# Optimization experiments

Hardware: AMD Instinct MI355X
Metric: run time of the kernel (lower is better)

The kernel has to match this reference:

```python
import jax, jax.numpy as jnp
import numpy as np

# NF4 16-level codebook (bitsandbytes values)
NF4_CODEBOOK = jnp.array([
    -1.0, -0.6961928009986877, -0.5250730514526367, -0.39491748809814453,
    -0.28444138169288635, -0.18477343022823334, -0.09105003625154495, 0.0,
    0.07958029955625534, 0.16093020141124725, 0.24611230194568634,
    0.33791524171829224, 0.44070982933044434, 0.5626170039176941,
    0.7229568362236328, 1.0], dtype=jnp.float32)

GROUP = 64      # quant_group_size for NF4
R = 16          # LoRA rank
ALPHA = 16      # lora_alpha -> scaling = ALPHA / R = 1.0
E, H, I, T, TOPK = 8, 2048, 1024, 512, 2


def nf4_dequant_gkn(packed, scales, K, N):
    """packed: [E, K//2, N] uint8-valued ints (two 4-bit codes per byte along K).
    scales: [E, K//GROUP, N] float32 per-group absmax. Returns [E, K, N] fp32."""
    e = packed.shape[0]
    lo = packed & 15
    hi = (packed >> 4) & 15
    codes = jnp.stack([lo, hi], axis=2).reshape(e, K, N)      # interleave along K
    w = NF4_CODEBOOK[codes]                                    # [E, K, N]
    w = w.reshape(e, K // GROUP, GROUP, N) * scales[:, :, None, :]
    return w.reshape(e, K, N)


def setup_inputs() -> dict:
    key = jax.random.key(0)
    ks = jax.random.split(key, 16)
    lora_std = 1.0 / np.sqrt(H)
    return {
        "x": jax.random.normal(ks[0], (T, H), jnp.float32),
        "topk_idx": jax.random.randint(ks[1], (T, TOPK), 0, E, jnp.int32),
        "topk_w": jax.random.uniform(ks[2], (T, TOPK), jnp.float32),
        "gate_packed": jax.random.randint(ks[3], (E, H // 2, I), 0, 256, jnp.int32),
        "gate_scales": jax.random.uniform(ks[4], (E, H // GROUP, I), jnp.float32) * 0.02,
        "up_packed": jax.random.randint(ks[5], (E, H // 2, I), 0, 256, jnp.int32),
        "up_scales": jax.random.uniform(ks[6], (E, H // GROUP, I), jnp.float32) * 0.02,
        "down_packed": jax.random.randint(ks[7], (E, I // 2, H), 0, 256, jnp.int32),
        "down_scales": jax.random.uniform(ks[8], (E, I // GROUP, H), jnp.float32) * 0.02,
        "gate_A": jax.random.normal(ks[9], (E, H, R), jnp.float32) * lora_std,
        "gate_B": jax.random.normal(ks[10], (E, R, I), jnp.float32) * 0.02,
        "up_A": jax.random.normal(ks[11], (E, H, R), jnp.float32) * lora_std,
        "up_B": jax.random.normal(ks[12], (E, R, I), jnp.float32) * 0.02,
        "down_A": jax.random.normal(ks[13], (E, I, R), jnp.float32) * lora_std,
        "down_B": jax.random.normal(ks[14], (E, R, H), jnp.float32) * 0.02,
    }


def reference(x, topk_idx, topk_w, gate_packed, gate_scales, up_packed, up_scales,
              down_packed, down_scales, gate_A, gate_B, up_A, up_B, down_A, down_B):
    scaling = ALPHA / R
    # Dequantized NF4 base + LoRA delta, GKN layout [E, K, N]
    Wg = nf4_dequant_gkn(gate_packed, gate_scales, H, I) + scaling * jnp.einsum('ekr,ern->ekn', gate_A, gate_B)
    Wu = nf4_dequant_gkn(up_packed, up_scales, H, I) + scaling * jnp.einsum('ekr,ern->ekn', up_A, up_B)
    Wd = nf4_dequant_gkn(down_packed, down_scales, I, H) + scaling * jnp.einsum('ekr,ern->ekn', down_A, down_B)
    # Grouped GEMM (dense-over-experts reference): SwiGLU per expert
    g = jnp.einsum('th,ehi->eti', x, Wg)          # [E, T, I]
    u = jnp.einsum('th,ehi->eti', x, Wu)
    h = jax.nn.silu(g) * u
    o = jnp.einsum('eti,eih->eth', h, Wd)         # [E, T, H]
    # Routing combine: per-token per-expert weight from top-k assignments
    w_te = jnp.sum((topk_idx[:, :, None] == jnp.arange(E)) * topk_w[:, :, None], axis=1)  # [T, E]
    return jnp.einsum('eth,te->th', o, w_te)
```

## Files before the change

kernel.cpp:

```cpp
#include <hip/hip_runtime.h>
#include <math.h>

#define NE 8
#define NH 2048
#define NI 1024
#define NT 512
#define NTOPK 2
#define NR 16
#define NGROUP 64
#define NPAIR (NT*NTOPK)

#define SPG 1040
#define SPD 528

typedef short bf16x8 __attribute__((ext_vector_type(8)));
typedef float f32x16 __attribute__((ext_vector_type(16)));
typedef unsigned int u32;

#define MFMA32 __builtin_amdgcn_mfma_f32_32x32x16_bf16

__device__ const float NF4_TAB[16] = {
    -1.0f, -0.6961928009986877f, -0.5250730514526367f, -0.39491748809814453f,
    -0.28444138169288635f, -0.18477343022823334f, -0.09105003625154495f, 0.0f,
    0.07958029955625534f, 0.16093020141124725f, 0.24611230194568634f,
    0.33791524171829224f, 0.44070982933044434f, 0.5626170039176941f,
    0.7229568362236328f, 1.0f};

#define OFF_EXPOFF 0
#define OFF_TOK    256
#define OFF_EXP    4352
#define OFF_W      8448
#define OFF_XAG    12544
#define OFF_XAU    45312
#define OFF_HA     78080
#define OFF_XCT    131072
#define OFF_GU     4325376
#define OFF_HBUF   8519680
#define OFF_HT     10616832
#define OFF_CG     12713984
#define OFF_CU     21233664
#define OFF_CD     29753344

__device__ inline u32 f2bf(float f) {
    return (__float_as_uint(f) + 0x8000u) >> 16;
}
__device__ inline u32 bfpack2(float a, float b) {
    return ((__float_as_uint(a) + 0x8000u) >> 16) |
           ((__float_as_uint(b) + 0x8000u) & 0xFFFF0000u);
}
__device__ inline bf16x8 asbf(uint4 w) {
    union { uint4 u; bf16x8 b; } c; c.u = w; return c.b;
}
__device__ inline bf16x8 bfzero() { return asbf(make_uint4(0,0,0,0)); }
__device__ inline float bf2f(u32 v) { return __uint_as_float(v << 16); }

__device__ __forceinline__ void stage16(const void* g, void* l) {
    __builtin_amdgcn_global_load_lds(
        (const __attribute__((address_space(1))) u32*)g,
        (__attribute__((address_space(3))) u32*)l, 16, 0, 0);
}
#define WAITV0()  asm volatile("s_waitcnt vmcnt(0)" ::: "memory")

__global__ __launch_bounds__(256) void k_cmp(const u32* __restrict__ in,
                                             unsigned char* __restrict__ out,
                                             int K2, int N, int SP) {
    __shared__ unsigned char tile[32][33];
    int e = blockIdx.z;
    int kp0 = blockIdx.y * 32, c0 = blockIdx.x * 32;
    const u32* ip = in + (size_t)e * K2 * N + (size_t)kp0 * N + c0;
    int tid = threadIdx.x;
    int r = tid >> 5, c = tid & 31;
    #pragma unroll
    for (int i = 0; i < 4; ++i)
        tile[r + 8 * i][c] = (unsigned char)ip[(size_t)(r + 8 * i) * N + c];
    __syncthreads();
    int col = tid >> 3, seg = tid & 7;
    u32 w = (u32)tile[seg * 4 + 0][col] | ((u32)tile[seg * 4 + 1][col] << 8) |
            ((u32)tile[seg * 4 + 2][col] << 16) |
            ((u32)tile[seg * 4 + 3][col] << 24);
    *(u32*)(out + (size_t)e * N * SP + (size_t)(c0 + col) * SP + kp0 + seg * 4) = w;
}

__global__ __launch_bounds__(1024) void k_route(const int* __restrict__ idx,
                                                const float* __restrict__ w,
                                                int* expert_off, int* ptok,
                                                int* pexp, float* pw) {
    __shared__ int cnt[NE], off[NE + 1], cur[NE];
    int tid = threadIdx.x;
    if (tid < NE) cnt[tid] = 0;
    __syncthreads();
    int e = idx[tid];
    float wt = w[tid];
    int t = tid >> 1;
    atomicAdd(&cnt[e], 1);
    __syncthreads();
    if (tid == 0) {
        off[0] = 0;
        for (int i = 0; i < NE; i++) off[i + 1] = off[i] + cnt[i];
    }
    __syncthreads();
    if (tid < NE) cur[tid] = off[tid];
    __syncthreads();
    int pos = atomicAdd(&cur[e], 1);
    ptok[pos] = t; pexp[pos] = e; pw[pos] = wt;
    if (tid <= NE) expert_off[tid] = off[tid];
}

__global__ __launch_bounds__(256) void k_xg(const float* __restrict__ x,
                                            const int* __restrict__ ptok,
                                            unsigned short* __restrict__ xcT) {
    int p = blockIdx.x;
    int t = ptok[p];
    int k = threadIdx.x * 8;
    const float* xr = x + (size_t)t * NH + k;
    float4 v0 = *(const float4*)xr;
    float4 v1 = *(const float4*)(xr + 4);
    uint4 w;
    w.x = bfpack2(v0.x, v0.y); w.y = bfpack2(v0.z, v0.w);
    w.z = bfpack2(v1.x, v1.y); w.w = bfpack2(v1.z, v1.w);
    *(uint4*)(xcT + ((size_t)(k >> 3) * NPAIR + p) * 8) = w;
}

__global__ __launch_bounds__(256) void k_xA(const float* __restrict__ x,
                                            const float* __restrict__ gA,
                                            const float* __restrict__ uA,
                                            const int* __restrict__ ptok,
                                            const int* __restrict__ pexp,
                                            unsigned short* __restrict__ xAg,
                                            unsigned short* __restrict__ xAu) {
    int p = blockIdx.x;
    int t = ptok[p], e = pexp[p];
    int tid = threadIdx.x;
    int r = tid & 15, ch = tid >> 4;
    const float* xr = x + (size_t)t * NH;
    const float* gAr = gA + (size_t)e * NH * NR;
    const float* uAr = uA + (size_t)e * NH * NR;
    float sg = 0.f, su = 0.f;
    for (int j = ch * 128; j < ch * 128 + 128; ++j) {
        float xv = xr[j];
        sg += xv * gAr[j * NR + r];
        su += xv * uAr[j * NR + r];
    }
    __shared__ float red[2][16][16];
    red[0][ch][r] = sg; red[1][ch][r] = su;
    __syncthreads();
    for (int st = 8; st >= 1; st >>= 1) {
        if (ch < st) {
            red[0][ch][r] += red[0][ch + st][r];
            red[1][ch][r] += red[1][ch + st][r];
        }
        __syncthreads();
    }
    if (tid < 16) {
        xAg[p * NR + tid] = (unsigned short)f2bf(red[0][0][tid]);
        xAu[p * NR + tid] = (unsigned short)f2bf(red[1][0][tid]);
    }
}

__global__ __launch_bounds__(64, 3) void k_gu(
    const unsigned short* __restrict__ xcT,
    const unsigned char* __restrict__ cgp, const float* __restrict__ gsc,
    const unsigned char* __restrict__ cup, const float* __restrict__ usc,
    const float* __restrict__ gB, const float* __restrict__ uB,
    const unsigned short* __restrict__ xAg, const unsigned short* __restrict__ xAu,
    const int* __restrict__ expert_off,
    unsigned short* __restrict__ gu)
{
    __shared__ u32 lut[256];
    __shared__ float sclb[32][32];

    int lane = threadIdx.x;
    int q = lane >> 5, cw = lane & 31;
    for (int i = lane; i < 256; i += 64)
        lut[i] = bfpack2(NF4_TAB[i & 15], NF4_TAB[(i >> 4) & 15]);

    int e = blockIdx.x;
    int c0 = blockIdx.y * 32;
    int mat = blockIdx.z & 1;
    int rt = blockIdx.z >> 1;
    const unsigned char* cp = mat ? cup : cgp;
    const float* scp = mat ? usc : gsc;
    const float* Bp = mat ? uB : gB;
    const unsigned short* xA = mat ? xAu : xAg;

    int off = expert_off[e];
    int cnt = expert_off[e + 1] - off;
    int colg = c0 + cw;

    {
        const float* sg = scp + (size_t)e * (NH / NGROUP) * NI + c0;
        #pragma unroll
        for (int g = 0; g < 4; ++g)
            stage16(sg + (size_t)(g * 8 + (lane >> 3)) * NI + ((lane & 7) << 2),
                    &sclb[g * 8][0]);
    }
    WAITV0();

    const unsigned char* cb = cp + ((size_t)e * NI + colg) * SPG + (q << 4);

    const int NS = NH / 64;
    for (int s0 = rt * 32; s0 < cnt; s0 += 128) {
        int rr = s0 + cw; if (rr > cnt - 1) rr = cnt - 1;
        int prow = off + rr;

        auto loadC = [&](uint4& c, int s) {
            c = *(const uint4*)(cb + (s << 5));
        };
        auto loadA = [&](bf16x8* d, int s) {
            #pragma unroll
            for (int ks = 0; ks < 4; ++ks)
                d[ks] = *(const bf16x8*)(xcT +
                            ((size_t)((s << 3) + (q << 2) + ks) * NPAIR + prow) * 8);
        };

        uint4 C0, C1;
        bf16x8 Aa[4], Ab[4];
        f32x16 acc;
        #pragma unroll
        for (int i = 0; i < 16; ++i) acc[i] = 0.f;

        auto compute = [&](const uint4& cv, const bf16x8* Ar, float scl) {
            const u32* cd = &cv.x;
            f32x16 t;
            #pragma unroll
            for (int i = 0; i < 16; ++i) t[i] = 0.f;
            #pragma unroll
            for (int ks = 0; ks < 4; ++ks) {
                u32 d = cd[ks];
                uint4 w4;
                w4.x = lut[d & 255];
                w4.y = lut[(d >> 8) & 255];
                w4.z = lut[(d >> 16) & 255];
                w4.w = lut[d >> 24];
                t = MFMA32(Ar[ks], asbf(w4), t, 0, 0, 0);
            }
            #pragma unroll
            for (int i = 0; i < 16; ++i) acc[i] += scl * t[i];
        };

        loadC(C0, 0); loadA(Aa, 0);
        loadC(C1, 1); loadA(Ab, 1);
        for (int s = 0; s < NS; s += 2) {
            compute(C0, Aa, sclb[s][cw]);
            if (s + 2 < NS) { loadC(C0, s + 2); loadA(Aa, s + 2); }
            compute(C1, Ab, sclb[s + 1][cw]);
            if (s + 3 < NS) { loadC(C1, s + 3); loadA(Ab, s + 3); }
        }

        {
            bf16x8 la = bfzero();
            if (s0 + cw < cnt)
                la = *(const bf16x8*)(xA + (size_t)(off + s0 + cw) * NR + (q << 3));
            const float* Bq = Bp + ((size_t)e * NR + (q << 3)) * NI + colg;
            uint4 w4; u32* wp = &w4.x;
            #pragma unroll
            for (int i = 0; i < 4; ++i)
                wp[i] = bfpack2(Bq[(2 * i) * NI], Bq[(2 * i + 1) * NI]);
            acc = MFMA32(la, asbf(w4), acc, 0, 0, 0);
        }
        unsigned short* outb = gu + (size_t)mat * NPAIR * NI;
        #pragma unroll
        for (int reg = 0; reg < 16; ++reg) {
            int rloc = (reg & 3) + 8 * (reg >> 2) + (q << 2);
            if (s0 + rloc < cnt)
                outb[(size_t)(off + s0 + rloc) * NI + colg] =
                    (unsigned short)f2bf(acc[reg]);
        }
    }
}

__global__ __launch_bounds__(256) void k_swiglu(const unsigned short* __restrict__ gu,
                                                unsigned short* __restrict__ hbuf,
                                                unsigned short* __restrict__ hT) {
    int i = (blockIdx.x * 256 + threadIdx.x) * 8;
    int p = i >> 10;
    int k0 = i & 1023;
    uint4 gv = *(const uint4*)(gu + i);
    uint4 uv = *(const uint4*)(gu + (size_t)NPAIR * NI + i);
    const u32* gp = &gv.x; const u32* up = &uv.x;
    uint4 hv; u32* hp = &hv.x;
    #pragma unroll
    for (int j = 0; j < 4; ++j) {
        float g0 = bf2f(gp[j] & 0xFFFFu), g1 = bf2f(gp[j] >> 16);
        float u0 = bf2f(up[j] & 0xFFFFu), u1 = bf2f(up[j] >> 16);
        float h0 = g0 * u0 / (1.f + __expf(-g0));
        float h1 = g1 * u1 / (1.f + __expf(-g1));
        hp[j] = bfpack2(h0, h1);
    }
    *(uint4*)(hbuf + i) = hv;
    *(uint4*)(hT + ((size_t)(k0 >> 3) * NPAIR + p) * 8) = hv;
}

__global__ __launch_bounds__(256) void k_hA(const unsigned short* __restrict__ hbuf,
                                            const float* __restrict__ dA,
                                            const int* __restrict__ pexp,
                                            unsigned short* __restrict__ hA) {
    int p = blockIdx.x;
    int e = pexp[p];
    int tid = threadIdx.x;
    int r = tid & 15, ch = tid >> 4;
    const unsigned short* hr = hbuf + (size_t)p * NI;
    const float* dAr = dA + (size_t)e * NI * NR;
    float sv = 0.f;
    for (int j = ch * 64; j < ch * 64 + 64; ++j) {
        float hv = bf2f(hr[j]);
        sv += hv * dAr[j * NR + r];
    }
    __shared__ float red[16][16];
    red[ch][r] = sv;
    __syncthreads();
    for (int st = 8; st >= 1; st >>= 1) {
        if (ch < st) red[ch][r] += red[ch + st][r];
        __syncthreads();
    }
    if (tid < 16) hA[p * NR + tid] = (unsigned short)f2bf(red[0][tid]);
}

__global__ __launch_bounds__(64, 3) void k_dn(
    const unsigned short* __restrict__ hT,
    const unsigned char* __restrict__ cdp, const float* __restrict__ dsc,
    const float* __restrict__ dB,
    const unsigned short* __restrict__ hA,
    const int* __restrict__ expert_off, const int* __restrict__ ptok,
    const float* __restrict__ pw,
    float* __restrict__ out)
{
    __shared__ u32 lut[256];
    __shared__ float sclb[16][32];

    int lane = threadIdx.x;
    int q = lane >> 5, cw = lane & 31;
    for (int i = lane; i < 256; i += 64)
        lut[i] = bfpack2(NF4_TAB[i & 15], NF4_TAB[(i >> 4) & 15]);

    int e = blockIdx.x;
    int c0 = blockIdx.y * 32;
    int rt = blockIdx.z;

    int off = expert_off[e];
    int cnt = expert_off[e + 1] - off;
    int colg = c0 + cw;

    {
        const float* sg = dsc + (size_t)e * (NI / NGROUP) * NH + c0;
        #pragma unroll
        for (int g = 0; g < 2; ++g)
            stage16(sg + (size_t)(g * 8 + (lane >> 3)) * NH + ((lane & 7) << 2),
                    &sclb[g * 8][0]);
    }
    WAITV0();

    const unsigned char* cb = cdp + ((size_t)e * NH + colg) * SPD + (q << 4);

    const int NS = NI / 64;
    for (int s0 = rt * 32; s0 < cnt; s0 += 128) {
        int rr = s0 + cw; if (rr > cnt - 1) rr = cnt - 1;
        int prow = off + rr;

        auto loadC = [&](uint4& c, int s) {
            c = *(const uint4*)(cb + (s << 5));
        };
        auto loadA = [&](bf16x8* d, int s) {
            #pragma unroll
            for (int ks = 0; ks < 4; ++ks)
                d[ks] = *(const bf16x8*)(hT +
                            ((size_t)((s << 3) + (q << 2) + ks) * NPAIR + prow) * 8);
        };

        uint4 C0, C1;
        bf16x8 Aa[4], Ab[4];
        f32x16 acc;
        #pragma unroll
        for (int i = 0; i < 16; ++i) acc[i] = 0.f;

        auto compute = [&](const uint4& cv, const bf16x8* Ar, float scl) {
            const u32* cd = &cv.x;
            f32x16 t;
            #pragma unroll
            for (int i = 0; i < 16; ++i) t[i] = 0.f;
            #pragma unroll
            for (int ks = 0; ks < 4; ++ks) {
                u32 d = cd[ks];
                uint4 w4;
                w4.x = lut[d & 255];
                w4.y = lut[(d >> 8) & 255];
                w4.z = lut[(d >> 16) & 255];
                w4.w = lut[d >> 24];
                t = MFMA32(Ar[ks], asbf(w4), t, 0, 0, 0);
            }
            #pragma unroll
            for (int i = 0; i < 16; ++i) acc[i] += scl * t[i];
        };

        loadC(C0, 0); loadA(Aa, 0);
        loadC(C1, 1); loadA(Ab, 1);
        for (int s = 0; s < NS; s += 2) {
            compute(C0, Aa, sclb[s][cw]);
            if (s + 2 < NS) { loadC(C0, s + 2); loadA(Aa, s + 2); }
            compute(C1, Ab, sclb[s + 1][cw]);
            if (s + 3 < NS) { loadC(C1, s + 3); loadA(Ab, s + 3); }
        }

        {
            bf16x8 la = bfzero();
            if (s0 + cw < cnt)
                la = *(const bf16x8*)(hA + (size_t)(off + s0 + cw) * NR + (q << 3));
            const float* Bq = dB + ((size_t)e * NR + (q << 3)) * NH + colg;
            uint4 w4; u32* wp = &w4.x;
            #pragma unroll
            for (int i = 0; i < 4; ++i)
                wp[i] = bfpack2(Bq[(2 * i) * NH], Bq[(2 * i + 1) * NH]);
            acc = MFMA32(la, asbf(w4), acc, 0, 0, 0);
        }
        #pragma unroll
        for (int reg = 0; reg < 16; ++reg) {
            int rloc = (reg & 3) + 8 * (reg >> 2) + (q << 2);
            if (s0 + rloc < cnt) {
                int p = off + s0 + rloc;
                atomicAdd(&out[(size_t)ptok[p] * NH + colg], acc[reg] * pw[p]);
            }
        }
    }
}

extern "C" void kernel_launch(void* const* d_in, const int* in_sizes, int n_in,
                              void* d_out, int out_size, void* d_ws,
                              size_t ws_size, hipStream_t stream) {
    const float* x = (const float*)d_in[0];
    const int* topk_idx = (const int*)d_in[1];
    const float* topk_w = (const float*)d_in[2];
    const int* gate_packed = (const int*)d_in[3];
    const float* gate_scales = (const float*)d_in[4];
    const int* up_packed = (const int*)d_in[5];
    const float* up_scales = (const float*)d_in[6];
    const int* down_packed = (const int*)d_in[7];
    const float* down_scales = (const float*)d_in[8];
    const float* gate_A = (const float*)d_in[9];
    const float* gate_B = (const float*)d_in[10];
    const float* up_A = (const float*)d_in[11];
    const float* up_B = (const float*)d_in[12];
    const float* down_A = (const float*)d_in[13];
    const float* down_B = (const float*)d_in[14];
    float* out = (float*)d_out;

    char* ws = (char*)d_ws;
    int* expert_off = (int*)(ws + OFF_EXPOFF);
    int* ptok = (int*)(ws + OFF_TOK);
    int* pexp = (int*)(ws + OFF_EXP);
    float* pw = (float*)(ws + OFF_W);
    unsigned short* xAg = (unsigned short*)(ws + OFF_XAG);
    unsigned short* xAu = (unsigned short*)(ws + OFF_XAU);
    unsigned short* hA = (unsigned short*)(ws + OFF_HA);
    unsigned short* xcT = (unsigned short*)(ws + OFF_XCT);
    unsigned short* gu = (unsigned short*)(ws + OFF_GU);
    unsigned short* hbuf = (unsigned short*)(ws + OFF_HBUF);
    unsigned short* hT = (unsigned short*)(ws + OFF_HT);
    unsigned char* cg = (unsigned char*)(ws + OFF_CG);
    unsigned char* cu = (unsigned char*)(ws + OFF_CU);
    unsigned char* cd = (unsigned char*)(ws + OFF_CD);

    hipMemsetAsync(d_out, 0, (size_t)NT * NH * sizeof(float), stream);

    k_cmp<<<dim3(NI / 32, (NH / 2) / 32, NE), 256, 0, stream>>>(
        (const u32*)gate_packed, cg, NH / 2, NI, SPG);
    k_cmp<<<dim3(NI / 32, (NH / 2) / 32, NE), 256, 0, stream>>>(
        (const u32*)up_packed, cu, NH / 2, NI, SPG);
    k_cmp<<<dim3(NH / 32, (NI / 2) / 32, NE), 256, 0, stream>>>(
        (const u32*)down_packed, cd, NI / 2, NH, SPD);

    k_route<<<1, 1024, 0, stream>>>(topk_idx, topk_w, expert_off, ptok, pexp, pw);
    k_xg<<<NPAIR, 256, 0, stream>>>(x, ptok, xcT);
    k_xA<<<NPAIR, 256, 0, stream>>>(x, gate_A, up_A, ptok, pexp, xAg, xAu);
    k_gu<<<dim3(NE, NI / 32, 8), 64, 0, stream>>>(
        xcT, cg, gate_scales, cu, up_scales, gate_B, up_B,
        xAg, xAu, expert_off, gu);
    k_swiglu<<<(NPAIR * NI) / (256 * 8), 256, 0, stream>>>(gu, hbuf, hT);
    k_hA<<<NPAIR, 256, 0, stream>>>(hbuf, down_A, pexp, hA);
    k_dn<<<dim3(NE, NH / 32, 4), 64, 0, stream>>>(
        hT, cd, down_scales, down_B, hA, expert_off, ptok, pw, out);
}
```

Before: 263.2 us.

## Process two 32-row tiles per wave to reuse dequantized NF4 weights

After: 269.2 us. 2.3% more time.

```diff
diff --git a/kernel.cpp b/kernel.cpp
--- a/kernel.cpp
+++ b/kernel.cpp
@@ -61,11 +61,19 @@
 }
 #define WAITV0()  asm volatile("s_waitcnt vmcnt(0)" ::: "memory")
 
-__global__ __launch_bounds__(256) void k_cmp(const u32* __restrict__ in,
-                                             unsigned char* __restrict__ out,
+__global__ __launch_bounds__(256) void k_cmp(const u32* __restrict__ in0,
+                                             const u32* __restrict__ in1,
+                                             unsigned char* __restrict__ out0,
+                                             unsigned char* __restrict__ out1,
                                              int K2, int N, int SP) {
     __shared__ unsigned char tile[32][33];
-    int e = blockIdx.z;
+    int z = blockIdx.z;
+    int e, which;
+    const u32* in; unsigned char* out;
+    if (in1) { e = z >> 1; which = z & 1; }
+    else     { e = z;      which = 0; }
+    in  = which ? in1  : in0;
+    out = which ? out1 : out0;
     int kp0 = blockIdx.y * 32, c0 = blockIdx.x * 32;
     const u32* ip = in + (size_t)e * K2 * N + (size_t)kp0 * N + c0;
     int tid = threadIdx.x;
@@ -157,7 +165,7 @@
     }
 }
 
-__global__ __launch_bounds__(64, 3) void k_gu(
+__global__ __launch_bounds__(64, 2) void k_gu(
     const unsigned short* __restrict__ xcT,
     const unsigned char* __restrict__ cgp, const float* __restrict__ gsc,
     const unsigned char* __restrict__ cup, const float* __restrict__ usc,
@@ -199,14 +207,15 @@
     const unsigned char* cb = cp + ((size_t)e * NI + colg) * SPG + (q << 4);
 
     const int NS = NH / 64;
-    for (int s0 = rt * 32; s0 < cnt; s0 += 128) {
-        int rr = s0 + cw; if (rr > cnt - 1) rr = cnt - 1;
-        int prow = off + rr;
+    for (int s0 = rt * 64; s0 < cnt; s0 += 128) {
+        int rr0 = s0 + cw;      if (rr0 > cnt - 1) rr0 = cnt - 1;
+        int rr1 = s0 + 32 + cw; if (rr1 > cnt - 1) rr1 = cnt - 1;
+        int prow0 = off + rr0, prow1 = off + rr1;
 
         auto loadC = [&](uint4& c, int s) {
             c = *(const uint4*)(cb + (s << 5));
         };
-        auto loadA = [&](bf16x8* d, int s) {
+        auto loadA = [&](bf16x8* d, int s, int prow) {
             #pragma unroll
             for (int ks = 0; ks < 4; ++ks)
                 d[ks] = *(const bf16x8*)(xcT +
@@ -214,16 +223,17 @@
         };
 
         uint4 C0, C1;
-        bf16x8 Aa[4], Ab[4];
-        f32x16 acc;
+        bf16x8 Aa0[4], Aa1[4], Ab0[4], Ab1[4];
+        f32x16 acc0, acc1;
         #pragma unroll
-        for (int i = 0; i < 16; ++i) acc[i] = 0.f;
-
-        auto compute = [&](const uint4& cv, const bf16x8* Ar, float scl) {
+        for (int i = 0; i < 16; ++i) { acc0[i] = 0.f; acc1[i] = 0.f; }
+
+        auto computeStep = [&](const uint4& cv, const bf16x8* A0,
+                               const bf16x8* A1, float scl) {
             const u32* cd = &cv.x;
-            f32x16 t;
-            #pragma unroll
-            for (int i = 0; i < 16; ++i) t[i] = 0.f;
+            f32x16 t0, t1;
+            #pragma unroll
+            for (int i = 0; i < 16; ++i) { t0[i] = 0.f; t1[i] = 0.f; }
             #pragma unroll
             for (int ks = 0; ks < 4; ++ks) {
                 u32 d = cd[ks];
@@ -232,31 +242,44 @@
                 w4.y = lut[(d >> 8) & 255];
                 w4.z = lut[(d >> 16) & 255];
                 w4.w = lut[d >> 24];
-                t = MFMA32(Ar[ks], asbf(w4), t, 0, 0, 0);
-            }
-            #pragma unroll
-            for (int i = 0; i < 16; ++i) acc[i] += scl * t[i];
+                t0 = MFMA32(A0[ks], asbf(w4), t0, 0, 0, 0);
+                t1 = MFMA32(A1[ks], asbf(w4), t1, 0, 0, 0);
+            }
+            #pragma unroll
+            for (int i = 0; i < 16; ++i) {
+                acc0[i] += scl * t0[i];
+                acc1[i] += scl * t1[i];
+            }
         };
 
-        loadC(C0, 0); loadA(Aa, 0);
-        loadC(C1, 1); loadA(Ab, 1);
+        loadC(C0, 0); loadA(Aa0, 0, prow0); loadA(Aa1, 0, prow1);
+        loadC(C1, 1); loadA(Ab0, 1, prow0); loadA(Ab1, 1, prow1);
         for (int s = 0; s < NS; s += 2) {
-            compute(C0, Aa, sclb[s][cw]);
-            if (s + 2 < NS) { loadC(C0, s + 2); loadA(Aa, s + 2); }
-            compute(C1, Ab, sclb[s + 1][cw]);
-            if (s + 3 < NS) { loadC(C1, s + 3); loadA(Ab, s + 3); }
+            computeStep(C0, Aa0, Aa1, sclb[s][cw]);
+            if (s + 2 < NS) {
+                loadC(C0, s + 2);
+                loadA(Aa0, s + 2, prow0); loadA(Aa1, s + 2, prow1);
+            }
+            computeStep(C1, Ab0, Ab1, sclb[s + 1][cw]);
+            if (s + 3 < NS) {
+                loadC(C1, s + 3);
+                loadA(Ab0, s + 3, prow0); loadA(Ab1, s + 3, prow1);
+            }
         }
 
         {
-            bf16x8 la = bfzero();
+            bf16x8 la0 = bfzero(), la1 = bfzero();
             if (s0 + cw < cnt)
-                la = *(const bf16x8*)(xA + (size_t)(off + s0 + cw) * NR + (q << 3));
+                la0 = *(const bf16x8*)(xA + (size_t)(off + s0 + cw) * NR + (q << 3));
+            if (s0 + 32 + cw < cnt)
+                la1 = *(const bf16x8*)(xA + (size_t)(off + s0 + 32 + cw) * NR + (q << 3));
             const float* Bq = Bp + ((size_t)e * NR + (q << 3)) * NI + colg;
             uint4 w4; u32* wp = &w4.x;
             #pragma unroll
             for (int i = 0; i < 4; ++i)
                 wp[i] = bfpack2(Bq[(2 * i) * NI], Bq[(2 * i + 1) * NI]);
-            acc = MFMA32(la, asbf(w4), acc, 0, 0, 0);
+            acc0 = MFMA32(la0, asbf(w4), acc0, 0, 0, 0);
+            acc1 = MFMA32(la1, asbf(w4), acc1, 0, 0, 0);
         }
         unsigned short* outb = gu + (size_t)mat * NPAIR * NI;
         #pragma unroll
@@ -264,7 +287,10 @@
             int rloc = (reg & 3) + 8 * (reg >> 2) + (q << 2);
             if (s0 + rloc < cnt)
                 outb[(size_t)(off + s0 + rloc) * NI + colg] =
-                    (unsigned short)f2bf(acc[reg]);
+                    (unsigned short)f2bf(acc0[reg]);
+            if (s0 + 32 + rloc < cnt)
+                outb[(size_t)(off + s0 + 32 + rloc) * NI + colg] =
+                    (unsigned short)f2bf(acc1[reg]);
         }
     }
 }
@@ -316,7 +342,7 @@
     if (tid < 16) hA[p * NR + tid] = (unsigned short)f2bf(red[0][tid]);
 }
 
-__global__ __launch_bounds__(64, 3) void k_dn(
+__global__ __launch_bounds__(64, 2) void k_dn(
     const unsigned short* __restrict__ hT,
     const unsigned char* __restrict__ cdp, const float* __restrict__ dsc,
     const float* __restrict__ dB,
@@ -353,14 +379,15 @@
     const unsigned char* cb = cdp + ((size_t)e * NH + colg) * SPD + (q << 4);
 
     const int NS = NI / 64;
-    for (int s0 = rt * 32; s0 < cnt; s0 += 128) {
-        int rr = s0 + cw; if (rr > cnt - 1) rr = cnt - 1;
-        int prow = off + rr;
+    for (int s0 = rt * 64; s0 < cnt; s0 += 128) {
+        int rr0 = s0 + cw;      if (rr0 > cnt - 1) rr0 = cnt - 1;
+        int rr1 = s0 + 32 + cw; if (rr1 > cnt - 1) rr1 = cnt - 1;
+        int prow0 = off + rr0, prow1 = off + rr1;
 
         auto loadC = [&](uint4& c, int s) {
             c = *(const uint4*)(cb + (s << 5));
         };
-        auto loadA = [&](bf16x8* d, int s) {
+        auto loadA = [&](bf16x8* d, int s, int prow) {
             #pragma unroll
             for (int ks = 0; ks < 4; ++ks)
                 d[ks] = *(const bf16x8*)(hT +
@@ -368,16 +395,17 @@
         };
 
         uint4 C0, C1;
-        bf16x8 Aa[4], Ab[4];
-        f32x16 acc;
+        bf16x8 Aa0[4], Aa1[4], Ab0[4], Ab1[4];
+        f32x16 acc0, acc1;
         #pragma unroll
-        for (int i = 0; i < 16; ++i) acc[i] = 0.f;
-
-        auto compute = [&](const uint4& cv, const bf16x8* Ar, float scl) {
+        for (int i = 0; i < 16; ++i) { acc0[i] = 0.f; acc1[i] = 0.f; }
+
+        auto computeStep = [&](const uint4& cv, const bf16x8* A0,
+                               const bf16x8* A1, float scl) {
             const u32* cd = &cv.x;
-            f32x16 t;
-            #pragma unroll
-            for (int i = 0; i < 16; ++i) t[i] = 0.f;
+            f32x16 t0, t1;
+            #pragma unroll
+            for (int i = 0; i < 16; ++i) { t0[i] = 0.f; t1[i] = 0.f; }
             #pragma unroll
             for (int ks = 0; ks < 4; ++ks) {
                 u32 d = cd[ks];
@@ -386,38 +414,55 @@
                 w4.y = lut[(d >> 8) & 255];
                 w4.z = lut[(d >> 16) & 255];
                 w4.w = lut[d >> 24];
-                t = MFMA32(Ar[ks], asbf(w4), t, 0, 0, 0);
-            }
-            #pragma unroll
-            for (int i = 0; i < 16; ++i) acc[i] += scl * t[i];
+                t0 = MFMA32(A0[ks], asbf(w4), t0, 0, 0, 0);
+                t1 = MFMA32(A1[ks], asbf(w4), t1, 0, 0, 0);
+            }
+            #pragma unroll
+            for (int i = 0; i < 16; ++i) {
+                acc0[i] += scl * t0[i];
+                acc1[i] += scl * t1[i];
+            }
         };
 
-        loadC(C0, 0); loadA(Aa, 0);
-        loadC(C1, 1); loadA(Ab, 1);
+        loadC(C0, 0); loadA(Aa0, 0, prow0); loadA(Aa1, 0, prow1);
+        loadC(C1, 1); loadA(Ab0, 1, prow0); loadA(Ab1, 1, prow1);
         for (int s = 0; s < NS; s += 2) {
-            compute(C0, Aa, sclb[s][cw]);
-            if (s + 2 < NS) { loadC(C0, s + 2); loadA(Aa, s + 2); }
-            compute(C1, Ab, sclb[s + 1][cw]);
-            if (s + 3 < NS) { loadC(C1, s + 3); loadA(Ab, s + 3); }
+            computeStep(C0, Aa0, Aa1, sclb[s][cw]);
+            if (s + 2 < NS) {
+                loadC(C0, s + 2);
+                loadA(Aa0, s + 2, prow0); loadA(Aa1, s + 2, prow1);
+            }
+            computeStep(C1, Ab0, Ab1, sclb[s + 1][cw]);
+            if (s + 3 < NS) {
+                loadC(C1, s + 3);
+                loadA(Ab0, s + 3, prow0); loadA(Ab1, s + 3, prow1);
+            }
         }
 
         {
-            bf16x8 la = bfzero();
+            bf16x8 la0 = bfzero(), la1 = bfzero();
             if (s0 + cw < cnt)
-                la = *(const bf16x8*)(hA + (size_t)(off + s0 + cw) * NR + (q << 3));
+                la0 = *(const bf16x8*)(hA + (size_t)(off + s0 + cw) * NR + (q << 3));
+            if (s0 + 32 + cw < cnt)
+                la1 = *(const bf16x8*)(hA + (size_t)(off + s0 + 32 + cw) * NR + (q << 3));
             const float* Bq = dB + ((size_t)e * NR + (q << 3)) * NH + colg;
             uint4 w4; u32* wp = &w4.x;
             #pragma unroll
             for (int i = 0; i < 4; ++i)
                 wp[i] = bfpack2(Bq[(2 * i) * NH], Bq[(2 * i + 1) * NH]);
-            acc = MFMA32(la, asbf(w4), acc, 0, 0, 0);
+            acc0 = MFMA32(la0, asbf(w4), acc0, 0, 0, 0);
+            acc1 = MFMA32(la1, asbf(w4), acc1, 0, 0, 0);
         }
         #pragma unroll
         for (int reg = 0; reg < 16; ++reg) {
             int rloc = (reg & 3) + 8 * (reg >> 2) + (q << 2);
             if (s0 + rloc < cnt) {
                 int p = off + s0 + rloc;
-                atomicAdd(&out[(size_t)ptok[p] * NH + colg], acc[reg] * pw[p]);
+                atomicAdd(&out[(size_t)ptok[p] * NH + colg], acc0[reg] * pw[p]);
+            }
+            if (s0 + 32 + rloc < cnt) {
+                int p = off + s0 + 32 + rloc;
+                atomicAdd(&out[(size_t)ptok[p] * NH + colg], acc1[reg] * pw[p]);
             }
         }
     }
@@ -461,21 +506,20 @@
 
     hipMemsetAsync(d_out, 0, (size_t)NT * NH * sizeof(float), stream);
 
-    k_cmp<<<dim3(NI / 32, (NH / 2) / 32, NE), 256, 0, stream>>>(
-        (const u32*)gate_packed, cg, NH / 2, NI, SPG);
-    k_cmp<<<dim3(NI / 32, (NH / 2) / 32, NE), 256, 0, stream>>>(
-        (const u32*)up_packed, cu, NH / 2, NI, SPG);
+    k_cmp<<<dim3(NI / 32, (NH / 2) / 32, 2 * NE), 256, 0, stream>>>(
+        (const u32*)gate_packed, (const u32*)up_packed, cg, cu, NH / 2, NI, SPG);
     k_cmp<<<dim3(NH / 32, (NI / 2) / 32, NE), 256, 0, stream>>>(
-        (const u32*)down_packed, cd, NI / 2, NH, SPD);
+        (const u32*)down_packed, (const u32*)nullptr, cd, (unsigned char*)nullptr,
+        NI / 2, NH, SPD);
 
     k_route<<<1, 1024, 0, stream>>>(topk_idx, topk_w, expert_off, ptok, pexp, pw);
     k_xg<<<NPAIR, 256, 0, stream>>>(x, ptok, xcT);
     k_xA<<<NPAIR, 256, 0, stream>>>(x, gate_A, up_A, ptok, pexp, xAg, xAu);
-    k_gu<<<dim3(NE, NI / 32, 8), 64, 0, stream>>>(
+    k_gu<<<dim3(NE, NI / 32, 4), 64, 0, stream>>>(
         xcT, cg, gate_scales, cu, up_scales, gate_B, up_B,
         xAg, xAu, expert_off, gu);
     k_swiglu<<<(NPAIR * NI) / (256 * 8), 256, 0, stream>>>(gu, hbuf, hT);
     k_hA<<<NPAIR, 256, 0, stream>>>(hbuf, down_A, pexp, hA);
-    k_dn<<<dim3(NE, NH / 32, 4), 64, 0, stream>>>(
+    k_dn<<<dim3(NE, NH / 32, 2), 64, 0, stream>>>(
         hT, cd, down_scales, down_B, hA, expert_off, ptok, pw, out);
 }
```

## Fuse NF4 repack kernels and routing into one launch with wider tiles

Applied to the files above, without the earlier changes.

After: 262.7 us. No clear change (-0.2%).

```diff
diff --git a/kernel.cpp b/kernel.cpp
--- a/kernel.cpp
+++ b/kernel.cpp
@@ -61,49 +61,89 @@
 }
 #define WAITV0()  asm volatile("s_waitcnt vmcnt(0)" ::: "memory")
 
-__global__ __launch_bounds__(256) void k_cmp(const u32* __restrict__ in,
-                                             unsigned char* __restrict__ out,
-                                             int K2, int N, int SP) {
-    __shared__ unsigned char tile[32][33];
-    int e = blockIdx.z;
-    int kp0 = blockIdx.y * 32, c0 = blockIdx.x * 32;
+__global__ __launch_bounds__(256) void k_cmp3(const u32* __restrict__ gin,
+                                              const u32* __restrict__ uin,
+                                              const u32* __restrict__ din,
+                                              unsigned char* __restrict__ cg,
+                                              unsigned char* __restrict__ cu,
+                                              unsigned char* __restrict__ cd,
+                                              const int* __restrict__ idx,
+                                              const float* __restrict__ w,
+                                              int* expert_off, int* ptok,
+                                              int* pexp, float* pw) {
+    __shared__ u32 tile32[32][33];
+    __shared__ int cnt[NE], off2[NE + 1], cur[NE];
+    int tid = threadIdx.x;
+    int z = blockIdx.z;
+
+    if (z == 24) {
+        if (blockIdx.x || blockIdx.y) return;
+        if (tid < NE) cnt[tid] = 0;
+        __syncthreads();
+        int e4[4]; float w4[4];
+        #pragma unroll
+        for (int i = 0; i < 4; ++i) {
+            int pr = tid * 4 + i;
+            e4[i] = idx[pr]; w4[i] = w[pr];
+            atomicAdd(&cnt[e4[i]], 1);
+        }
+        __syncthreads();
+        if (tid == 0) {
+            off2[0] = 0;
+            for (int i = 0; i < NE; i++) off2[i + 1] = off2[i] + cnt[i];
+        }
+        __syncthreads();
+        if (tid < NE) cur[tid] = off2[tid];
+        __syncthreads();
+        #pragma unroll
+        for (int i = 0; i < 4; ++i) {
+            int pr = tid * 4 + i;
+            int pos = atomicAdd(&cur[e4[i]], 1);
+            ptok[pos] = pr >> 1; pexp[pos] = e4[i]; pw[pos] = w4[i];
+        }
+        if (tid <= NE) expert_off[tid] = off2[tid];
+        return;
+    }
+
+    const u32* in; unsigned char* out; int K2, N, SP, e;
+    if (z < 2 * NE) {
+        e = z >> 1;
+        in = (z & 1) ? uin : gin; out = (z & 1) ? cu : cg;
+        K2 = NH / 2; N = NI; SP = SPG;
+        if ((int)blockIdx.x >= N / 128) return;
+    } else {
+        e = z - 2 * NE;
+        in = din; out = cd;
+        K2 = NI / 2; N = NH; SP = SPD;
+        if ((int)blockIdx.y >= K2 / 32) return;
+    }
+    int kp0 = blockIdx.y * 32, c0 = blockIdx.x * 128;
+
+    int c16 = tid & 31, rr = tid >> 5;
     const u32* ip = in + (size_t)e * K2 * N + (size_t)kp0 * N + c0;
-    int tid = threadIdx.x;
-    int r = tid >> 5, c = tid & 31;
     #pragma unroll
-    for (int i = 0; i < 4; ++i)
-        tile[r + 8 * i][c] = (unsigned char)ip[(size_t)(r + 8 * i) * N + c];
+    for (int pass = 0; pass < 4; ++pass) {
+        int r = pass * 8 + rr;
+        uint4 v = *(const uint4*)(ip + (size_t)r * N + c16 * 4);
+        tile32[r][c16] = (v.x & 255) | ((v.y & 255) << 8) |
+                         ((v.z & 255) << 16) | ((v.w & 255) << 24);
+    }
     __syncthreads();
-    int col = tid >> 3, seg = tid & 7;
-    u32 w = (u32)tile[seg * 4 + 0][col] | ((u32)tile[seg * 4 + 1][col] << 8) |
-            ((u32)tile[seg * 4 + 2][col] << 16) |
-            ((u32)tile[seg * 4 + 3][col] << 24);
-    *(u32*)(out + (size_t)e * N * SP + (size_t)(c0 + col) * SP + kp0 + seg * 4) = w;
-}
-
-__global__ __launch_bounds__(1024) void k_route(const int* __restrict__ idx,
-                                                const float* __restrict__ w,
-                                                int* expert_off, int* ptok,
-                                                int* pexp, float* pw) {
-    __shared__ int cnt[NE], off[NE + 1], cur[NE];
-    int tid = threadIdx.x;
-    if (tid < NE) cnt[tid] = 0;
-    __syncthreads();
-    int e = idx[tid];
-    float wt = w[tid];
-    int t = tid >> 1;
-    atomicAdd(&cnt[e], 1);
-    __syncthreads();
-    if (tid == 0) {
-        off[0] = 0;
-        for (int i = 0; i < NE; i++) off[i + 1] = off[i] + cnt[i];
-    }
-    __syncthreads();
-    if (tid < NE) cur[tid] = off[tid];
-    __syncthreads();
-    int pos = atomicAdd(&cur[e], 1);
-    ptok[pos] = t; pexp[pos] = e; pw[pos] = wt;
-    if (tid <= NE) expert_off[tid] = off[tid];
+
+    int col = tid >> 1, half = tid & 1;
+    int cq = col >> 2, sh = (col & 3) * 8;
+    uint4 ow; u32* op = &ow.x;
+    #pragma unroll
+    for (int i = 0; i < 4; ++i) {
+        int base = half * 16 + i * 4;
+        u32 b0 = (tile32[base + 0][cq] >> sh) & 255;
+        u32 b1 = (tile32[base + 1][cq] >> sh) & 255;
+        u32 b2 = (tile32[base + 2][cq] >> sh) & 255;
+        u32 b3 = (tile32[base + 3][cq] >> sh) & 255;
+        op[i] = b0 | (b1 << 8) | (b2 << 16) | (b3 << 24);
+    }
+    *(uint4*)(out + (size_t)e * N * SP + (size_t)(c0 + col) * SP
+              + kp0 + half * 16) = ow;
 }
 
 __global__ __launch_bounds__(256) void k_xg(const float* __restrict__ x,
@@ -461,14 +501,10 @@
 
     hipMemsetAsync(d_out, 0, (size_t)NT * NH * sizeof(float), stream);
 
-    k_cmp<<<dim3(NI / 32, (NH / 2) / 32, NE), 256, 0, stream>>>(
-        (const u32*)gate_packed, cg, NH / 2, NI, SPG);
-    k_cmp<<<dim3(NI / 32, (NH / 2) / 32, NE), 256, 0, stream>>>(
-        (const u32*)up_packed, cu, NH / 2, NI, SPG);
-    k_cmp<<<dim3(NH / 32, (NI / 2) / 32, NE), 256, 0, stream>>>(
-        (const u32*)down_packed, cd, NI / 2, NH, SPD);
-
-    k_route<<<1, 1024, 0, stream>>>(topk_idx, topk_w, expert_off, ptok, pexp, pw);
+    k_cmp3<<<dim3(16, 32, 25), 256, 0, stream>>>(
+        (const u32*)gate_packed, (const u32*)up_packed, (const u32*)down_packed,
+        cg, cu, cd, topk_idx, topk_w, expert_off, ptok, pexp, pw);
+
     k_xg<<<NPAIR, 256, 0, stream>>>(x, ptok, xcT);
     k_xA<<<NPAIR, 256, 0, stream>>>(x, gate_A, up_A, ptok, pexp, xAg, xAu);
     k_gu<<<dim3(NE, NI / 32, 8), 64, 0, stream>>>(
```
